# Optimization experiments

Measured on AMD Instinct MI355X. Metric: run time of the kernel, lower is better.

Reference implementation:

```python
import jax, jax.numpy as jnp
import numpy as np

DT = 1e-4  # integration step, matches Model(dt=0.0001)
T = 4_000_000


def setup_inputs() -> dict:
    key = jax.random.key(0)
    ks = jax.random.split(key, 8)
    inputs = jax.random.normal(ks[0], (1, T, 3), dtype=jnp.float32)
    # time column made increasing (as in a real signal record)
    t = jnp.arange(T, dtype=jnp.float32) * DT
    inputs = inputs.at[0, :, 0].set(t)
    # small-scale 2x2 system matrices; A shifted toward -0.5*I so the
    # 4M-step linear recurrence is stable (no overflow over long horizons)
    A = -0.5 * jnp.eye(2, dtype=jnp.float32) + 0.05 * jax.random.normal(ks[1], (2, 2), jnp.float32)
    B = 0.1 * jax.random.normal(ks[2], (2, 2), jnp.float32)
    D = 0.1 * jax.random.normal(ks[3], (2, 2), jnp.float32)
    E = 0.1 * jax.random.normal(ks[4], (2, 2), jnp.float32)
    cov_in = 0.1 * jax.random.normal(ks[5], (2, 2), jnp.float32)
    training_params = jax.random.normal(ks[6], (1, 2), jnp.float32)
    initial_states = jnp.zeros((1, 5), dtype=jnp.float32)
    return {"inputs": inputs, "A": A, "B": B, "D": D, "E": E,
            "cov_in": cov_in, "training_params": training_params,
            "initial_states": initial_states}


def reference(inputs, A, B, D, E, cov_in, training_params, initial_states):
    # Faithful to GRCell.call: cov = cov_in every step (new_cov is discarded),
    # so XiCov / XiCovC / transition matrix are time-invariant constants.
    dt = jnp.float32(DT)
    sqrt2 = jnp.sqrt(jnp.float32(2.0))
    x_signal = jnp.array([1.0, 0.0], dtype=inputs.dtype)
    XiCov = (E - cov_in @ B) / sqrt2                      # (2,2)
    XiCovC = XiCov @ (-sqrt2 * B.T)                       # (2,2)
    Trans = jnp.eye(2, dtype=inputs.dtype) + (A - XiCovC) * dt  # I + (A-XiCovC)dt
    Cout = -sqrt2 * B.T * dt                              # output map, (2,2)
    p0 = training_params[0, 0]
    p1 = training_params[0, 1]
    seq = inputs[0]                                       # [T, 3] = (time, dy1, dy2)

    def step(x, inp):
        t = inp[0]
        dy = inp[1:]
        out = Cout @ x                                    # emitted BEFORE update
        x_new = Trans @ x + XiCov @ dy + (p0 * jnp.cos(p1 * t) * dt) * x_signal
        return x_new, out

    x0 = initial_states[0, :2]
    _, outs = jax.lax.scan(step, x0, seq)                 # outs: [T, 2]
    return outs[None]                                     # [1, T, 2]
```

## Files before the change

### kernel.cpp

```cpp
#include <hip/hip_runtime.h>
#include <math.h>


constexpr int   TN    = 4000000;
constexpr float FDT   = 1e-4f;
constexpr int   L     = 16;
constexpr int   LOG2L = 4;
constexpr int   K     = TN / L;
constexpr int   BT    = 256;
constexpr int   NT    = (K + BT - 1) / BT;
constexpr int   ROWF4 = 9;
constexpr int   F4IN  = TN * 3 / 4;
constexpr int   F4OUT = TN * 2 / 4;

struct Consts {
  float T00, T01, T10, T11;
  float X00, X01, X10, X11;
  float C00, C01, C10, C11;
  float p0, p1;
};

__device__ inline Consts make_consts(const float* __restrict__ A,
                                     const float* __restrict__ B,
                                     const float* __restrict__ E,
                                     const float* __restrict__ cov,
                                     const float* __restrict__ tp) {
  const float s2 = 1.41421356237309515f;
  Consts c;
  float Xi[2][2];
  for (int i = 0; i < 2; ++i)
    for (int j = 0; j < 2; ++j)
      Xi[i][j] = (E[i*2+j] - (cov[i*2+0]*B[0*2+j] + cov[i*2+1]*B[1*2+j])) / s2;
  float XiC[2][2];
  for (int i = 0; i < 2; ++i)
    for (int j = 0; j < 2; ++j)
      XiC[i][j] = Xi[i][0]*(-s2*B[j*2+0]) + Xi[i][1]*(-s2*B[j*2+1]);
  c.T00 = 1.0f + (A[0] - XiC[0][0]) * FDT;
  c.T01 =        (A[1] - XiC[0][1]) * FDT;
  c.T10 =        (A[2] - XiC[1][0]) * FDT;
  c.T11 = 1.0f + (A[3] - XiC[1][1]) * FDT;
  c.X00 = Xi[0][0]; c.X01 = Xi[0][1]; c.X10 = Xi[1][0]; c.X11 = Xi[1][1];
  c.C00 = -s2 * B[0] * FDT;
  c.C01 = -s2 * B[2] * FDT;
  c.C10 = -s2 * B[1] * FDT;
  c.C11 = -s2 * B[3] * FDT;
  c.p0 = tp[0]; c.p1 = tp[1];
  return c;
}

__device__ inline void step(float& x0, float& x1, float t, float a, float b,
                            const Consts& c) {
  float u0 = fmaf(c.X00, a, fmaf(c.X01, b, c.p0 * __cosf(c.p1 * t) * FDT));
  float u1 = fmaf(c.X10, a, c.X11 * b);
  float n0 = fmaf(c.T00, x0, fmaf(c.T01, x1, u0));
  float n1 = fmaf(c.T10, x0, fmaf(c.T11, x1, u1));
  x0 = n0; x1 = n1;
}

__device__ inline void fsq(float* M) {
  float a = M[0]*M[0] + M[1]*M[2];
  float b = M[0]*M[1] + M[1]*M[3];
  float d = M[2]*M[0] + M[3]*M[2];
  float e = M[2]*M[1] + M[3]*M[3];
  M[0] = a; M[1] = b; M[2] = d; M[3] = e;
}

__device__ inline void fmm(const float* a, const float* b, float* o) {
  o[0] = a[0]*b[0] + a[1]*b[2];
  o[1] = a[0]*b[1] + a[1]*b[3];
  o[2] = a[2]*b[0] + a[3]*b[2];
  o[3] = a[2]*b[1] + a[3]*b[3];
}

__device__ inline void mulleft(const float* P, float* M) {
  float a0 = P[0]*M[0] + P[1]*M[2];
  float a1 = P[0]*M[1] + P[1]*M[3];
  float a2 = P[2]*M[0] + P[3]*M[2];
  float a3 = P[2]*M[1] + P[3]*M[3];
  M[0]=a0; M[1]=a1; M[2]=a2; M[3]=a3;
}

__device__ inline void pow_table(const Consts& c, float (*Pt)[4], int n) {
  float M[4] = {c.T00, c.T01, c.T10, c.T11};
  for (int s = 0; s < LOG2L; ++s) fsq(M);
  Pt[0][0] = M[0]; Pt[0][1] = M[1]; Pt[0][2] = M[2]; Pt[0][3] = M[3];
  for (int i = 1; i < n; ++i) {
    fsq(M);
    Pt[i][0] = M[0]; Pt[i][1] = M[1]; Pt[i][2] = M[2]; Pt[i][3] = M[3];
  }
}

__device__ inline void stage_tile(const float4* __restrict__ seq4, int tile,
                                  float4* __restrict__ ls, int tid) {
  const size_t base4 = (size_t)tile * 3072;
  #pragma unroll
  for (int it = 0; it < 4; ++it) {
    const int u = it * BT + tid;
    const size_t g = base4 + (size_t)(it * 768 + 3 * tid);
    float4 v0 = make_float4(0.f,0.f,0.f,0.f);
    float4 v1 = v0, v2 = v0;
    if (g     < (size_t)F4IN) v0 = seq4[g];
    if (g + 1 < (size_t)F4IN) v1 = seq4[g + 1];
    if (g + 2 < (size_t)F4IN) v2 = seq4[g + 2];
    const int st  = u >> 2;
    const int kq  = u & 3;
    const int rot = (st >> 3) & 7;
    float4* row = ls + st * ROWF4;
    row[(2*kq     + rot) & 7] = make_float4(v0.y, v0.z, v1.x, v1.y);
    row[(2*kq + 1 + rot) & 7] = make_float4(v1.w, v2.x, v2.z, v2.w);
  }
}

__global__ void __launch_bounds__(BT, 4)
k1(const float* __restrict__ seq, const float* __restrict__ A,
   const float* __restrict__ B, const float* __restrict__ E,
   const float* __restrict__ cov, const float* __restrict__ tp,
   float2* __restrict__ agg) {
  __shared__ float4 ls[BT * ROWF4];
  __shared__ float  wg[4][2];
  const int tid  = threadIdx.x;
  const int lane = tid & 63;
  const int w    = tid >> 6;
  const int tile = blockIdx.x;
  Consts c = make_consts(A, B, E, cov, tp);

  stage_tile((const float4*)seq, tile, ls, tid);
  __syncthreads();

  float Pt[7][4];
  pow_table(c, Pt, 7);

  float x0 = 0.f, x1 = 0.f;
  const float4* row = &ls[tid * ROWF4];
  const int rot = (tid >> 3) & 7;
  const int gstep = (tile * BT + tid) * L;
  #pragma unroll
  for (int q = 0; q < 8; ++q) {
    float4 d = row[(q + rot) & 7];
    step(x0, x1, (float)(gstep + 2*q)     * FDT, d.x, d.y, c);
    step(x0, x1, (float)(gstep + 2*q + 1) * FDT, d.z, d.w, c);
  }

  float v0 = x0, v1 = x1;
  #pragma unroll
  for (int s = 0; s < 6; ++s) {
    int st = 1 << s;
    float p0 = __shfl_up(v0, st);
    float p1 = __shfl_up(v1, st);
    if (lane >= st) {
      float n0 = fmaf(Pt[s][0], p0, fmaf(Pt[s][1], p1, v0));
      float n1 = fmaf(Pt[s][2], p0, fmaf(Pt[s][3], p1, v1));
      v0 = n0; v1 = n1;
    }
  }
  if (lane == 63) { wg[w][0] = v0; wg[w][1] = v1; }
  __syncthreads();
  if (tid == BT - 1) {
    float E0 = 0.f, E1 = 0.f;
    for (int ww = 0; ww < 3; ++ww) {
      float n0 = fmaf(Pt[6][0], E0, fmaf(Pt[6][1], E1, wg[ww][0]));
      float n1 = fmaf(Pt[6][2], E0, fmaf(Pt[6][3], E1, wg[ww][1]));
      E0 = n0; E1 = n1;
    }
    float a0 = fmaf(Pt[6][0], E0, fmaf(Pt[6][1], E1, v0));
    float a1 = fmaf(Pt[6][2], E0, fmaf(Pt[6][3], E1, v1));
    agg[tile] = make_float2(a0, a1);
  }
}

__global__ void __launch_bounds__(BT, 3)
k3(const float* __restrict__ seq, const float* __restrict__ A,
   const float* __restrict__ B, const float* __restrict__ E,
   const float* __restrict__ cov, const float* __restrict__ tp,
   const float* __restrict__ ini, const float2* __restrict__ agg,
   float* __restrict__ out) {
  __shared__ float4 ls[BT * ROWF4];
  __shared__ float  wg[4][2];
  __shared__ float  sY[2];
  const int tid  = threadIdx.x;
  const int lane = tid & 63;
  const int w    = tid >> 6;
  const int tile = blockIdx.x;
  Consts c = make_consts(A, B, E, cov, tp);

  stage_tile((const float4*)seq, tile, ls, tid);
  __syncthreads();

  float Pt[8][4];
  pow_table(c, Pt, 8);

  float x0 = 0.f, x1 = 0.f;
  float4* row = &ls[tid * ROWF4];
  const int rot = (tid >> 3) & 7;
  const int gstep = (tile * BT + tid) * L;
  #pragma unroll
  for (int q = 0; q < 8; ++q) {
    float4 d = row[(q + rot) & 7];
    step(x0, x1, (float)(gstep + 2*q)     * FDT, d.x, d.y, c);
    step(x0, x1, (float)(gstep + 2*q + 1) * FDT, d.z, d.w, c);
  }

  float v0 = x0, v1 = x1;
  #pragma unroll
  for (int s = 0; s < 6; ++s) {
    int st = 1 << s;
    float p0 = __shfl_up(v0, st);
    float p1 = __shfl_up(v1, st);
    if (lane >= st) {
      float n0 = fmaf(Pt[s][0], p0, fmaf(Pt[s][1], p1, v0));
      float n1 = fmaf(Pt[s][2], p0, fmaf(Pt[s][3], p1, v1));
      v0 = n0; v1 = n1;
    }
  }
  if (lane == 63) { wg[w][0] = v0; wg[w][1] = v1; }
  __syncthreads();
  float E0 = 0.f, E1 = 0.f;
  for (int ww = 0; ww < w; ++ww) {
    float n0 = fmaf(Pt[6][0], E0, fmaf(Pt[6][1], E1, wg[ww][0]));
    float n1 = fmaf(Pt[6][2], E0, fmaf(Pt[6][3], E1, wg[ww][1]));
    E0 = n0; E1 = n1;
  }
  float pv0 = __shfl_up(v0, 1);
  float pv1 = __shfl_up(v1, 1);
  if (lane == 0) { pv0 = 0.f; pv1 = 0.f; }
  float Ml[4] = {1.f,0.f,0.f,1.f};
  #pragma unroll
  for (int b = 0; b < 6; ++b) if ((lane >> b) & 1) mulleft(Pt[b], Ml);
  const float xe0 = fmaf(Ml[0], E0, fmaf(Ml[1], E1, pv0));
  const float xe1 = fmaf(Ml[2], E0, fmaf(Ml[3], E1, pv1));
  __syncthreads();

  float Q[4] = {Pt[7][0], Pt[7][1], Pt[7][2], Pt[7][3]};
  fsq(Q);
  float Q2[4], Q3[4], Q4[4];
  fmm(Q, Q, Q2); fmm(Q2, Q, Q3); fmm(Q2, Q2, Q4);
  float QW[7][4];
  for (int i = 0; i < 4; ++i) QW[0][i] = Q4[i];
  for (int s = 1; s < 7; ++s) fmm(QW[s-1], QW[s-1], QW[s]);

  float i0 = 0.f, i1 = 0.f;
  float inc[4][2];
  #pragma unroll
  for (int j = 0; j < 4; ++j) {
    int idx = 4 * tid + j;
    float e0 = 0.f, e1 = 0.f;
    if (idx == 0)      { e0 = ini[0]; e1 = ini[1]; }
    else if (idx < NT) { float2 a = agg[idx-1]; e0 = a.x; e1 = a.y; }
    float n0 = fmaf(Q[0], i0, fmaf(Q[1], i1, e0));
    float n1 = fmaf(Q[2], i0, fmaf(Q[3], i1, e1));
    i0 = n0; i1 = n1;
    inc[j][0] = i0; inc[j][1] = i1;
  }
  float s0 = i0, s1 = i1;
  #pragma unroll
  for (int s = 0; s < 6; ++s) {
    int st = 1 << s;
    float p0 = __shfl_up(s0, st);
    float p1 = __shfl_up(s1, st);
    if (lane >= st) {
      float n0 = fmaf(QW[s][0], p0, fmaf(QW[s][1], p1, s0));
      float n1 = fmaf(QW[s][2], p0, fmaf(QW[s][3], p1, s1));
      s0 = n0; s1 = n1;
    }
  }
  if (lane == 63) { wg[w][0] = s0; wg[w][1] = s1; }
  __syncthreads();
  float F0 = 0.f, F1 = 0.f;
  for (int ww = 0; ww < w; ++ww) {
    float n0 = fmaf(QW[6][0], F0, fmaf(QW[6][1], F1, wg[ww][0]));
    float n1 = fmaf(QW[6][2], F0, fmaf(QW[6][3], F1, wg[ww][1]));
    F0 = n0; F1 = n1;
  }
  float q0 = __shfl_up(s0, 1);
  float q1 = __shfl_up(s1, 1);
  if (lane == 0) { q0 = 0.f; q1 = 0.f; }
  float Mq[4] = {1.f,0.f,0.f,1.f};
  #pragma unroll
  for (int b = 0; b < 6; ++b) if ((lane >> b) & 1) mulleft(QW[b], Mq);
  float Eth0 = fmaf(Mq[0], F0, fmaf(Mq[1], F1, q0));
  float Eth1 = fmaf(Mq[2], F0, fmaf(Mq[3], F1, q1));
  {
    const float* Pj[4] = {Q, Q2, Q3, Q4};
    #pragma unroll
    for (int j = 0; j < 4; ++j) {
      int idx = 4 * tid + j;
      if (idx == tile) {
        sY[0] = fmaf(Pj[j][0], Eth0, fmaf(Pj[j][1], Eth1, inc[j][0]));
        sY[1] = fmaf(Pj[j][2], Eth0, fmaf(Pj[j][3], Eth1, inc[j][1]));
      }
    }
  }
  __syncthreads();

  float Mt[4] = {1.f,0.f,0.f,1.f};
  #pragma unroll
  for (int b = 0; b < 8; ++b) if ((tid >> b) & 1) mulleft(Pt[b], Mt);
  float y0 = sY[0], y1 = sY[1];
  x0 = fmaf(Mt[0], y0, fmaf(Mt[1], y1, xe0));
  x1 = fmaf(Mt[2], y0, fmaf(Mt[3], y1, xe1));

  #pragma unroll
  for (int q = 0; q < 8; ++q) {
    float4 d = row[(q + rot) & 7];
    float4 o;
    o.x = fmaf(c.C00, x0, c.C01 * x1); o.y = fmaf(c.C10, x0, c.C11 * x1);
    step(x0, x1, (float)(gstep + 2*q) * FDT, d.x, d.y, c);
    o.z = fmaf(c.C00, x0, c.C01 * x1); o.w = fmaf(c.C10, x0, c.C11 * x1);
    step(x0, x1, (float)(gstep + 2*q + 1) * FDT, d.z, d.w, c);
    row[(q + rot) & 7] = o;
  }
  __syncthreads();

  float4* out4 = (float4*)out;
  const size_t obase = (size_t)tile * 2048;
  #pragma unroll
  for (int i = 0; i < 8; ++i) {
    int lf = i * BT + tid;
    size_t g = obase + (size_t)lf;
    if (g < (size_t)F4OUT) {
      int cc = lf >> 3, s = lf & 7;
      int rc = (cc >> 3) & 7;
      out4[g] = ls[cc * ROWF4 + ((s + rc) & 7)];
    }
  }
}

extern "C" void kernel_launch(void* const* d_in, const int* in_sizes, int n_in,
                              void* d_out, int out_size, void* d_ws, size_t ws_size,
                              hipStream_t stream) {
  const float* seq = (const float*)d_in[0];
  const float* A   = (const float*)d_in[1];
  const float* B   = (const float*)d_in[2];
  const float* E   = (const float*)d_in[4];
  const float* cov = (const float*)d_in[5];
  const float* tp  = (const float*)d_in[6];
  const float* ini = (const float*)d_in[7];
  float* out = (float*)d_out;

  float2* agg = (float2*)d_ws;

  k1<<<NT, BT, 0, stream>>>(seq, A, B, E, cov, tp, agg);
  k3<<<NT, BT, 0, stream>>>(seq, A, B, E, cov, tp, ini, agg, out);
}
```

Measured before the change: 141.9 us.

## Replace k1 scan with register-resident weighted reduction and restructure k3 prefix

```diff
diff --git a/kernel.cpp b/kernel.cpp
--- a/kernel.cpp
+++ b/kernel.cpp
@@ -5,7 +5,6 @@
 constexpr int   TN    = 4000000;
 constexpr float FDT   = 1e-4f;
 constexpr int   L     = 16;
-constexpr int   LOG2L = 4;
 constexpr int   K     = TN / L;
 constexpr int   BT    = 256;
 constexpr int   NT    = (K + BT - 1) / BT;
@@ -65,13 +64,6 @@
   M[0] = a; M[1] = b; M[2] = d; M[3] = e;
 }
 
-__device__ inline void fmm(const float* a, const float* b, float* o) {
-  o[0] = a[0]*b[0] + a[1]*b[2];
-  o[1] = a[0]*b[1] + a[1]*b[3];
-  o[2] = a[2]*b[0] + a[3]*b[2];
-  o[3] = a[2]*b[1] + a[3]*b[3];
-}
-
 __device__ inline void mulleft(const float* P, float* M) {
   float a0 = P[0]*M[0] + P[1]*M[2];
   float a1 = P[0]*M[1] + P[1]*M[3];
@@ -80,13 +72,74 @@
   M[0]=a0; M[1]=a1; M[2]=a2; M[3]=a3;
 }
 
-__device__ inline void pow_table(const Consts& c, float (*Pt)[4], int n) {
-  float M[4] = {c.T00, c.T01, c.T10, c.T11};
-  for (int s = 0; s < LOG2L; ++s) fsq(M);
-  Pt[0][0] = M[0]; Pt[0][1] = M[1]; Pt[0][2] = M[2]; Pt[0][3] = M[3];
-  for (int i = 1; i < n; ++i) {
-    fsq(M);
-    Pt[i][0] = M[0]; Pt[i][1] = M[1]; Pt[i][2] = M[2]; Pt[i][3] = M[3];
+__device__ inline void powmat8(const float* M, int e, float* R) {
+  float C[4] = {M[0], M[1], M[2], M[3]};
+  R[0] = 1.f; R[1] = 0.f; R[2] = 0.f; R[3] = 1.f;
+  #pragma unroll
+  for (int b = 0; b < 8; ++b) {
+    if ((e >> b) & 1) mulleft(C, R);
+    fsq(C);
+  }
+}
+
+__global__ void __launch_bounds__(BT, 4)
+k1(const float* __restrict__ seq, const float* __restrict__ A,
+   const float* __restrict__ B, const float* __restrict__ E,
+   const float* __restrict__ cov, const float* __restrict__ tp,
+   float2* __restrict__ agg) {
+  __shared__ float wg[4][2];
+  const int tid  = threadIdx.x;
+  const int lane = tid & 63;
+  const int w    = tid >> 6;
+  const int tile = blockIdx.x;
+  Consts c = make_consts(A, B, E, cov, tp);
+
+  const float4* s4 = (const float4*)seq;
+  const size_t base = (size_t)tile * 3072 + 3 * tid;
+  const float4 z4 = make_float4(0.f, 0.f, 0.f, 0.f);
+  float4 v[12];
+  #pragma unroll
+  for (int it = 0; it < 4; ++it) {
+    size_t g = base + (size_t)(it * 768);
+    v[3*it+0] = (g     < (size_t)F4IN) ? s4[g]     : z4;
+    v[3*it+1] = (g + 1 < (size_t)F4IN) ? s4[g + 1] : z4;
+    v[3*it+2] = (g + 2 < (size_t)F4IN) ? s4[g + 2] : z4;
+  }
+
+  float S[4] = {c.T00, c.T01, c.T10, c.T11};
+  fsq(S); fsq(S);
+  float R[4];
+  powmat8(S, 255 - tid, R);
+  float S256[4] = {S[0], S[1], S[2], S[3]};
+  #pragma unroll
+  for (int i = 0; i < 8; ++i) fsq(S256);
+
+  float acc0 = 0.f, acc1 = 0.f;
+  #pragma unroll
+  for (int it = 3; it >= 0; --it) {
+    float x0 = 0.f, x1 = 0.f;
+    const float4 a = v[3*it], b = v[3*it+1], d = v[3*it+2];
+    const int st0 = tile * 4096 + 1024 * it + 4 * tid;
+    step(x0, x1, (float)(st0    ) * FDT, a.y, a.z, c);
+    step(x0, x1, (float)(st0 + 1) * FDT, b.x, b.y, c);
+    step(x0, x1, (float)(st0 + 2) * FDT, b.w, d.x, c);
+    step(x0, x1, (float)(st0 + 3) * FDT, d.z, d.w, c);
+    if (it != 3) mulleft(S256, R);
+    acc0 += R[0]*x0 + R[1]*x1;
+    acc1 += R[2]*x0 + R[3]*x1;
+  }
+
+  #pragma unroll
+  for (int m = 1; m < 64; m <<= 1) {
+    acc0 += __shfl_xor(acc0, m);
+    acc1 += __shfl_xor(acc1, m);
+  }
+  if (lane == 0) { wg[w][0] = acc0; wg[w][1] = acc1; }
+  __syncthreads();
+  if (tid == 0) {
+    float a0 = wg[0][0] + wg[1][0] + wg[2][0] + wg[3][0];
+    float a1 = wg[0][1] + wg[1][1] + wg[2][1] + wg[3][1];
+    agg[tile] = make_float2(a0, a1);
   }
 }
 
@@ -112,63 +165,6 @@
 }
 
 __global__ void __launch_bounds__(BT, 4)
-k1(const float* __restrict__ seq, const float* __restrict__ A,
-   const float* __restrict__ B, const float* __restrict__ E,
-   const float* __restrict__ cov, const float* __restrict__ tp,
-   float2* __restrict__ agg) {
-  __shared__ float4 ls[BT * ROWF4];
-  __shared__ float  wg[4][2];
-  const int tid  = threadIdx.x;
-  const int lane = tid & 63;
-  const int w    = tid >> 6;
-  const int tile = blockIdx.x;
-  Consts c = make_consts(A, B, E, cov, tp);
-
-  stage_tile((const float4*)seq, tile, ls, tid);
-  __syncthreads();
-
-  float Pt[7][4];
-  pow_table(c, Pt, 7);
-
-  float x0 = 0.f, x1 = 0.f;
-  const float4* row = &ls[tid * ROWF4];
-  const int rot = (tid >> 3) & 7;
-  const int gstep = (tile * BT + tid) * L;
-  #pragma unroll
-  for (int q = 0; q < 8; ++q) {
-    float4 d = row[(q + rot) & 7];
-    step(x0, x1, (float)(gstep + 2*q)     * FDT, d.x, d.y, c);
-    step(x0, x1, (float)(gstep + 2*q + 1) * FDT, d.z, d.w, c);
-  }
-
-  float v0 = x0, v1 = x1;
-  #pragma unroll
-  for (int s = 0; s < 6; ++s) {
-    int st = 1 << s;
-    float p0 = __shfl_up(v0, st);
-    float p1 = __shfl_up(v1, st);
-    if (lane >= st) {
-      float n0 = fmaf(Pt[s][0], p0, fmaf(Pt[s][1], p1, v0));
-      float n1 = fmaf(Pt[s][2], p0, fmaf(Pt[s][3], p1, v1));
-      v0 = n0; v1 = n1;
-    }
-  }
-  if (lane == 63) { wg[w][0] = v0; wg[w][1] = v1; }
-  __syncthreads();
-  if (tid == BT - 1) {
-    float E0 = 0.f, E1 = 0.f;
-    for (int ww = 0; ww < 3; ++ww) {
-      float n0 = fmaf(Pt[6][0], E0, fmaf(Pt[6][1], E1, wg[ww][0]));
-      float n1 = fmaf(Pt[6][2], E0, fmaf(Pt[6][3], E1, wg[ww][1]));
-      E0 = n0; E1 = n1;
-    }
-    float a0 = fmaf(Pt[6][0], E0, fmaf(Pt[6][1], E1, v0));
-    float a1 = fmaf(Pt[6][2], E0, fmaf(Pt[6][3], E1, v1));
-    agg[tile] = make_float2(a0, a1);
-  }
-}
-
-__global__ void __launch_bounds__(BT, 3)
 k3(const float* __restrict__ seq, const float* __restrict__ A,
    const float* __restrict__ B, const float* __restrict__ E,
    const float* __restrict__ cov, const float* __restrict__ tp,
@@ -184,120 +180,116 @@
   Consts c = make_consts(A, B, E, cov, tp);
 
   stage_tile((const float4*)seq, tile, ls, tid);
-  __syncthreads();
-
-  float Pt[8][4];
-  pow_table(c, Pt, 8);
-
-  float x0 = 0.f, x1 = 0.f;
+
+  {
+    float Qb[4] = {c.T00, c.T01, c.T10, c.T11};
+    #pragma unroll
+    for (int i = 0; i < 12; ++i) fsq(Qb);
+    float i0 = 0.f, i1 = 0.f;
+    float inc[4][2];
+    #pragma unroll
+    for (int j = 0; j < 4; ++j) {
+      int idx = 4 * tid + j;
+      float e0 = 0.f, e1 = 0.f;
+      if (idx == 0)      { e0 = ini[0]; e1 = ini[1]; }
+      else if (idx < NT) { float2 a = agg[idx-1]; e0 = a.x; e1 = a.y; }
+      float n0 = fmaf(Qb[0], i0, fmaf(Qb[1], i1, e0));
+      float n1 = fmaf(Qb[2], i0, fmaf(Qb[3], i1, e1));
+      i0 = n0; i1 = n1;
+      inc[j][0] = i0; inc[j][1] = i1;
+    }
+    float Q4[4] = {Qb[0], Qb[1], Qb[2], Qb[3]};
+    fsq(Q4); fsq(Q4);
+    float C[4] = {Q4[0], Q4[1], Q4[2], Q4[3]};
+    float v0 = i0, v1 = i1;
+    #pragma unroll
+    for (int s = 0; s < 6; ++s) {
+      int st = 1 << s;
+      float p0 = __shfl_up(v0, st);
+      float p1 = __shfl_up(v1, st);
+      if (lane >= st) {
+        float n0 = fmaf(C[0], p0, fmaf(C[1], p1, v0));
+        float n1 = fmaf(C[2], p0, fmaf(C[3], p1, v1));
+        v0 = n0; v1 = n1;
+      }
+      fsq(C);
+    }
+    if (lane == 63) { wg[w][0] = v0; wg[w][1] = v1; }
+    __syncthreads();
+    float F0 = 0.f, F1 = 0.f;
+    for (int ww = 0; ww < w; ++ww) {
+      float n0 = fmaf(C[0], F0, fmaf(C[1], F1, wg[ww][0]));
+      float n1 = fmaf(C[2], F0, fmaf(C[3], F1, wg[ww][1]));
+      F0 = n0; F1 = n1;
+    }
+    float q0 = __shfl_up(v0, 1);
+    float q1 = __shfl_up(v1, 1);
+    if (lane == 0) { q0 = 0.f; q1 = 0.f; }
+    float Mq[4];
+    powmat8(Q4, lane, Mq);
+    float Eth0 = fmaf(Mq[0], F0, fmaf(Mq[1], F1, q0));
+    float Eth1 = fmaf(Mq[2], F0, fmaf(Mq[3], F1, q1));
+    if (tid == (tile >> 2)) {
+      int j = tile & 3;
+      float Rj[4] = {Qb[0], Qb[1], Qb[2], Qb[3]};
+      for (int m = 0; m < j; ++m) mulleft(Qb, Rj);
+      sY[0] = fmaf(Rj[0], Eth0, fmaf(Rj[1], Eth1, inc[j][0]));
+      sY[1] = fmaf(Rj[2], Eth0, fmaf(Rj[3], Eth1, inc[j][1]));
+    }
+    __syncthreads();
+  }
+
+  float Pb[4] = {c.T00, c.T01, c.T10, c.T11};
+  #pragma unroll
+  for (int i = 0; i < 4; ++i) fsq(Pb);
   float4* row = &ls[tid * ROWF4];
   const int rot = (tid >> 3) & 7;
   const int gstep = (tile * BT + tid) * L;
-  #pragma unroll
-  for (int q = 0; q < 8; ++q) {
-    float4 d = row[(q + rot) & 7];
-    step(x0, x1, (float)(gstep + 2*q)     * FDT, d.x, d.y, c);
-    step(x0, x1, (float)(gstep + 2*q + 1) * FDT, d.z, d.w, c);
-  }
-
-  float v0 = x0, v1 = x1;
-  #pragma unroll
-  for (int s = 0; s < 6; ++s) {
-    int st = 1 << s;
-    float p0 = __shfl_up(v0, st);
-    float p1 = __shfl_up(v1, st);
-    if (lane >= st) {
-      float n0 = fmaf(Pt[s][0], p0, fmaf(Pt[s][1], p1, v0));
-      float n1 = fmaf(Pt[s][2], p0, fmaf(Pt[s][3], p1, v1));
-      v0 = n0; v1 = n1;
-    }
-  }
-  if (lane == 63) { wg[w][0] = v0; wg[w][1] = v1; }
-  __syncthreads();
-  float E0 = 0.f, E1 = 0.f;
-  for (int ww = 0; ww < w; ++ww) {
-    float n0 = fmaf(Pt[6][0], E0, fmaf(Pt[6][1], E1, wg[ww][0]));
-    float n1 = fmaf(Pt[6][2], E0, fmaf(Pt[6][3], E1, wg[ww][1]));
-    E0 = n0; E1 = n1;
-  }
-  float pv0 = __shfl_up(v0, 1);
-  float pv1 = __shfl_up(v1, 1);
-  if (lane == 0) { pv0 = 0.f; pv1 = 0.f; }
-  float Ml[4] = {1.f,0.f,0.f,1.f};
-  #pragma unroll
-  for (int b = 0; b < 6; ++b) if ((lane >> b) & 1) mulleft(Pt[b], Ml);
-  const float xe0 = fmaf(Ml[0], E0, fmaf(Ml[1], E1, pv0));
-  const float xe1 = fmaf(Ml[2], E0, fmaf(Ml[3], E1, pv1));
-  __syncthreads();
-
-  float Q[4] = {Pt[7][0], Pt[7][1], Pt[7][2], Pt[7][3]};
-  fsq(Q);
-  float Q2[4], Q3[4], Q4[4];
-  fmm(Q, Q, Q2); fmm(Q2, Q, Q3); fmm(Q2, Q2, Q4);
-  float QW[7][4];
-  for (int i = 0; i < 4; ++i) QW[0][i] = Q4[i];
-  for (int s = 1; s < 7; ++s) fmm(QW[s-1], QW[s-1], QW[s]);
-
-  float i0 = 0.f, i1 = 0.f;
-  float inc[4][2];
-  #pragma unroll
-  for (int j = 0; j < 4; ++j) {
-    int idx = 4 * tid + j;
-    float e0 = 0.f, e1 = 0.f;
-    if (idx == 0)      { e0 = ini[0]; e1 = ini[1]; }
-    else if (idx < NT) { float2 a = agg[idx-1]; e0 = a.x; e1 = a.y; }
-    float n0 = fmaf(Q[0], i0, fmaf(Q[1], i1, e0));
-    float n1 = fmaf(Q[2], i0, fmaf(Q[3], i1, e1));
-    i0 = n0; i1 = n1;
-    inc[j][0] = i0; inc[j][1] = i1;
-  }
-  float s0 = i0, s1 = i1;
-  #pragma unroll
-  for (int s = 0; s < 6; ++s) {
-    int st = 1 << s;
-    float p0 = __shfl_up(s0, st);
-    float p1 = __shfl_up(s1, st);
-    if (lane >= st) {
-      float n0 = fmaf(QW[s][0], p0, fmaf(QW[s][1], p1, s0));
-      float n1 = fmaf(QW[s][2], p0, fmaf(QW[s][3], p1, s1));
-      s0 = n0; s1 = n1;
-    }
-  }
-  if (lane == 63) { wg[w][0] = s0; wg[w][1] = s1; }
-  __syncthreads();
-  float F0 = 0.f, F1 = 0.f;
-  for (int ww = 0; ww < w; ++ww) {
-    float n0 = fmaf(QW[6][0], F0, fmaf(QW[6][1], F1, wg[ww][0]));
-    float n1 = fmaf(QW[6][2], F0, fmaf(QW[6][3], F1, wg[ww][1]));
-    F0 = n0; F1 = n1;
-  }
-  float q0 = __shfl_up(s0, 1);
-  float q1 = __shfl_up(s1, 1);
-  if (lane == 0) { q0 = 0.f; q1 = 0.f; }
-  float Mq[4] = {1.f,0.f,0.f,1.f};
-  #pragma unroll
-  for (int b = 0; b < 6; ++b) if ((lane >> b) & 1) mulleft(QW[b], Mq);
-  float Eth0 = fmaf(Mq[0], F0, fmaf(Mq[1], F1, q0));
-  float Eth1 = fmaf(Mq[2], F0, fmaf(Mq[3], F1, q1));
+  float xe0, xe1;
   {
-    const float* Pj[4] = {Q, Q2, Q3, Q4};
-    #pragma unroll
-    for (int j = 0; j < 4; ++j) {
-      int idx = 4 * tid + j;
-      if (idx == tile) {
-        sY[0] = fmaf(Pj[j][0], Eth0, fmaf(Pj[j][1], Eth1, inc[j][0]));
-        sY[1] = fmaf(Pj[j][2], Eth0, fmaf(Pj[j][3], Eth1, inc[j][1]));
+    float x0 = 0.f, x1 = 0.f;
+    #pragma unroll
+    for (int q = 0; q < 8; ++q) {
+      float4 d = row[(q + rot) & 7];
+      step(x0, x1, (float)(gstep + 2*q)     * FDT, d.x, d.y, c);
+      step(x0, x1, (float)(gstep + 2*q + 1) * FDT, d.z, d.w, c);
+    }
+    float C[4] = {Pb[0], Pb[1], Pb[2], Pb[3]};
+    float v0 = x0, v1 = x1;
+    #pragma unroll
+    for (int s = 0; s < 6; ++s) {
+      int st = 1 << s;
+      float p0 = __shfl_up(v0, st);
+      float p1 = __shfl_up(v1, st);
+      if (lane >= st) {
+        float n0 = fmaf(C[0], p0, fmaf(C[1], p1, v0));
+        float n1 = fmaf(C[2], p0, fmaf(C[3], p1, v1));
+        v0 = n0; v1 = n1;
       }
-    }
-  }
-  __syncthreads();
-
-  float Mt[4] = {1.f,0.f,0.f,1.f};
-  #pragma unroll
-  for (int b = 0; b < 8; ++b) if ((tid >> b) & 1) mulleft(Pt[b], Mt);
+      fsq(C);
+    }
+    if (lane == 63) { wg[w][0] = v0; wg[w][1] = v1; }
+    __syncthreads();
+    float E0 = 0.f, E1 = 0.f;
+    for (int ww = 0; ww < w; ++ww) {
+      float n0 = fmaf(C[0], E0, fmaf(C[1], E1, wg[ww][0]));
+      float n1 = fmaf(C[2], E0, fmaf(C[3], E1, wg[ww][1]));
+      E0 = n0; E1 = n1;
+    }
+    float pv0 = __shfl_up(v0, 1);
+    float pv1 = __shfl_up(v1, 1);
+    if (lane == 0) { pv0 = 0.f; pv1 = 0.f; }
+    float Ml[4];
+    powmat8(Pb, lane, Ml);
+    xe0 = fmaf(Ml[0], E0, fmaf(Ml[1], E1, pv0));
+    xe1 = fmaf(Ml[2], E0, fmaf(Ml[3], E1, pv1));
+  }
+
+  float Mt[4];
+  powmat8(Pb, tid, Mt);
   float y0 = sY[0], y1 = sY[1];
-  x0 = fmaf(Mt[0], y0, fmaf(Mt[1], y1, xe0));
-  x1 = fmaf(Mt[2], y0, fmaf(Mt[3], y1, xe1));
+  float x0 = fmaf(Mt[0], y0, fmaf(Mt[1], y1, xe0));
+  float x1 = fmaf(Mt[2], y0, fmaf(Mt[3], y1, xe1));
 
   #pragma unroll
   for (int q = 0; q < 8; ++q) {
```

Result: faster. 124.0 us (-12.6%).
